# Optimization experiments

Hardware: AMD Instinct MI355X
Metric: run time of the kernel (lower is better)

The kernel has to match this reference:

```python
import jax, jax.numpy as jnp
import numpy as np

HIDDEN_DIM = 256
N = 8192


def setup_inputs() -> dict:
    key = jax.random.key(0)
    k1, k2, k3, k4 = jax.random.split(key, 4)
    img = jax.random.normal(k1, (N, HIDDEN_DIM), dtype=jnp.float32)
    text = jax.random.normal(k2, (N, HIDDEN_DIM), dtype=jnp.float32)
    # nn.Linear(hidden_dim, hidden_dim, bias=False) weights, shape [out, in]
    scale = 1.0 / np.sqrt(HIDDEN_DIM)
    Wq = jax.random.uniform(k3, (HIDDEN_DIM, HIDDEN_DIM), dtype=jnp.float32, minval=-scale, maxval=scale)
    Wk = jax.random.uniform(k4, (HIDDEN_DIM, HIDDEN_DIM), dtype=jnp.float32, minval=-scale, maxval=scale)
    return {"img": img, "text": text, "Wq": Wq, "Wk": Wk}


def reference(img, text, Wq, Wk):
    d = img.shape[-1]
    norm_fact = 1.0 / jnp.sqrt(jnp.asarray(d, dtype=img.dtype))
    Q = img @ Wq.T                       # [N, D]
    K = text @ Wk.T                      # [N, D]
    scores = Q @ K.T                     # [N, N]
    # softmax over dim=1 (keys), then scaled by 1/sqrt(D)
    attn = jax.nn.softmax(scores, axis=1) * norm_fact
    out_img = attn @ img                 # [N, D]
    out_text = attn @ text               # [N, D]
    return (out_img, out_text)
```

## Files before the change

kernel.cpp:

```cpp
#include <hip/hip_runtime.h>

typedef unsigned short ushort_t;
typedef unsigned int uint_t;
typedef __attribute__((ext_vector_type(8))) short short8;
typedef __attribute__((ext_vector_type(8))) _Float16 half8;
typedef __attribute__((ext_vector_type(4))) _Float16 half4;
typedef __attribute__((ext_vector_type(4))) float float4v;

#define MFMA_BF16(a, b, c) __builtin_amdgcn_mfma_f32_16x16x32_bf16((a), (b), (c), 0, 0, 0)
#define MFMA_F16(a, b, c) __builtin_amdgcn_mfma_f32_16x16x32_f16((a), (b), (c), 0, 0, 0)

#define NQ 8192
#define DIM 256
#define DV 512

__device__ __forceinline__ ushort_t f2bf(float x) {
  union { float f; uint_t u; } v; v.f = x;
  return (ushort_t)((v.u + 0x7fffu + ((v.u >> 16) & 1u)) >> 16);
}
__device__ __forceinline__ float bf2f(ushort_t b) {
  union { uint_t u; float f; } v; v.u = ((uint_t)b) << 16;
  return v.f;
}

__device__ __forceinline__ half8 cvt8h(const float* p) {
  float4v a = *(const float4v*)p;
  float4v b = *(const float4v*)(p + 4);
  half8 r;
  r[0] = (_Float16)a[0]; r[1] = (_Float16)a[1];
  r[2] = (_Float16)a[2]; r[3] = (_Float16)a[3];
  r[4] = (_Float16)b[0]; r[5] = (_Float16)b[1];
  r[6] = (_Float16)b[2]; r[7] = (_Float16)b[3];
  return r;
}

__device__ __forceinline__ half8 as_h8(short8 s) {
  union { short8 s; half8 h; } u; u.s = s; return u.h;
}

__device__ __forceinline__ void load_lds_16(const void* g, void* l) {
  __builtin_amdgcn_global_load_lds(
      (const __attribute__((address_space(1))) uint_t*)g,
      (__attribute__((address_space(3))) uint_t*)l, 16, 0, 0);
}

__device__ __forceinline__ void barrier_vm0_lgkm0() {
  asm volatile("s_waitcnt vmcnt(0) lgkmcnt(0)\ns_barrier" ::: "memory");
}
__device__ __forceinline__ void barrier_lgkm0() {
  asm volatile("s_waitcnt lgkmcnt(0)\ns_barrier" ::: "memory");
}

__global__ __launch_bounds__(256, 2) void pre_kernel(
    const float* __restrict__ img, const float* __restrict__ text,
    const float* __restrict__ Wq, const float* __restrict__ Wk,
    _Float16* __restrict__ Qh, _Float16* __restrict__ Kh,
    ushort_t* __restrict__ Vt) {
  __shared__ float tile[64][65];
  const int bid = blockIdx.x;
  const int tid = threadIdx.x;
  if (bid < 1024) {
    const int bx = bid & 127;
    const int by = (bid >> 7) & 3;
    const int bz = bid >> 9;
    const int lane = tid & 63;
    const int wv = tid >> 6;
    const int l16 = lane & 15;
    const int quad = lane >> 4;
    const float* A = bz ? text : img;
    const float* W = bz ? Wk : Wq;
    _Float16* C = bz ? Kh : Qh;
    const int row = bx * 64 + wv * 16 + l16;
    const int colbase = by * 64;

    float4v acc[4];
#pragma unroll
    for (int c = 0; c < 4; ++c) acc[c] = (float4v){0.f, 0.f, 0.f, 0.f};
#pragma unroll
    for (int f = 0; f < 8; ++f) {
      const int k0 = f * 32 + quad * 8;
      half8 af = cvt8h(A + (size_t)row * DIM + k0);
#pragma unroll
      for (int c = 0; c < 4; ++c) {
        half8 bfr = cvt8h(W + (size_t)(colbase + c * 16 + l16) * DIM + k0);
        acc[c] = MFMA_F16(af, bfr, acc[c]);
      }
    }
    const int rbase = bx * 64 + wv * 16 + quad * 4;
#pragma unroll
    for (int c = 0; c < 4; ++c)
#pragma unroll
      for (int r = 0; r < 4; ++r)
        C[(size_t)(rbase + r) * DIM + colbase + c * 16 + l16] = (_Float16)acc[c][r];
  } else {
    const int vb = bid - 1024;
    const int n0 = (vb & 127) * 64;
    const int c0 = (vb >> 7) * 64;
    const float* src = (c0 < 256) ? img : text;
    const int cc0 = (c0 < 256) ? c0 : (c0 - 256);
#pragma unroll
    for (int i = 0; i < 4; ++i) {
      const int r = i * 16 + (tid >> 4);
      const int c = (tid & 15) * 4;
      *(float4v*)&tile[r][c] = *(const float4v*)(src + (size_t)(n0 + r) * DIM + cc0 + c);
    }
    __syncthreads();
    const int c = tid >> 2;
    const int seg = tid & 3;
    ushort_t tmp[16];
#pragma unroll
    for (int t = 0; t < 16; ++t) tmp[t] = f2bf(tile[seg * 16 + t][c]);
    ushort_t* dst = Vt + (size_t)(c0 + c) * NQ + n0 + seg * 16;
    *(short8*)dst = *(short8*)&tmp[0];
    *(short8*)(dst + 8) = *(short8*)&tmp[8];
  }
}

__device__ __forceinline__ void stage_K(const _Float16* __restrict__ Kh, int k0,
                                        ushort_t* dst, int tid, int wv) {
#pragma unroll
  for (int i = 0; i < 4; ++i) {
    const int chunk = i * 256 + tid;
    const int n = chunk >> 5;
    const int cs = (chunk & 31) ^ (n & 7);
    load_lds_16(Kh + (size_t)(k0 + n) * DIM + cs * 8,
                (char*)dst + (i * 256 + wv * 64) * 16);
  }
}
__device__ __forceinline__ void stage_V(const ushort_t* __restrict__ Vt, int k0,
                                        ushort_t* dst, int tid, int wv) {
#pragma unroll
  for (int i = 0; i < 8; ++i) {
    const int chunk = i * 256 + tid;
    const int vrow = chunk >> 2;
    const int dc = (chunk & 3) ^ ((vrow >> 1) & 3);
    load_lds_16(Vt + (size_t)vrow * NQ + k0 + dc * 8,
                (char*)dst + (i * 256 + wv * 64) * 16);
  }
}

__global__ __launch_bounds__(256, 2) void attn_kernel(
    const _Float16* __restrict__ Qh, const _Float16* __restrict__ Kh,
    const ushort_t* __restrict__ Vt, _Float16* __restrict__ pacc,
    float* __restrict__ pdenom, int kps, int ks) {
  extern __shared__ __align__(16) ushort_t smem[];
  ushort_t* ldsV = smem + 16384;

  const int tid = threadIdx.x;
  const int lane = tid & 63;
  const int wv = tid >> 6;
  const int l16 = lane & 15;
  const int quad = lane >> 4;
  const int id = blockIdx.x;
  const int split = id & (ks - 1);
  const int qtile = id / ks;
  const int kbeg = split * kps;
  const int sw2 = (l16 >> 1) & 3;
  const int swk = l16 & 7;

  short8 qf[8];
  {
    const _Float16* qptr = Qh + (size_t)(qtile * 64 + wv * 16 + l16) * DIM;
#pragma unroll
    for (int f = 0; f < 8; ++f)
      qf[f] = *(const short8*)(qptr + f * 32 + quad * 8);
  }

  float4v acc[4][8];
#pragma unroll
  for (int m = 0; m < 4; ++m)
#pragma unroll
    for (int c = 0; c < 8; ++c) acc[m][c] = (float4v){0.f, 0.f, 0.f, 0.f};
  float dacc[4] = {0.f, 0.f, 0.f, 0.f};

  const int ntiles = kps >> 5;

  stage_K(Kh, kbeg, smem, tid, wv);
  stage_V(Vt, kbeg, ldsV, tid, wv);

  for (int t = 0; t < ntiles; ++t) {
    const ushort_t* Kt = smem + (t & 1) * 8192;
    barrier_vm0_lgkm0();
    if (t + 1 < ntiles)
      stage_K(Kh, kbeg + (t + 1) * 32, smem + ((t + 1) & 1) * 8192, tid, wv);

    if (t > 0) {
      const ushort_t* Pprev = smem + 32768 + ((t - 1) & 1) * 2048;
      short8 pa[4];
#pragma unroll
      for (int m = 0; m < 4; ++m)
        pa[m] = *(const short8*)(Pprev + (m * 16 + l16) * 32 + (quad ^ sw2) * 8);
#pragma unroll
      for (int c = 0; c < 8; ++c) {
        const int vcol = (wv * 8 + c) * 16 + l16;
        short8 vb = *(const short8*)(ldsV + vcol * 32 + (quad ^ sw2) * 8);
#pragma unroll
        for (int m = 0; m < 4; ++m)
          acc[m][c] = MFMA_BF16(pa[m], vb, acc[m][c]);
      }
    }

    float4v s0 = (float4v){0.f, 0.f, 0.f, 0.f};
    float4v s1 = (float4v){0.f, 0.f, 0.f, 0.f};
#pragma unroll
    for (int f = 0; f < 8; ++f) {
      const int cs = ((f * 4 + quad) ^ swk) * 8;
      short8 kb0 = *(const short8*)(Kt + l16 * DIM + cs);
      short8 kb1 = *(const short8*)(Kt + (l16 + 16) * DIM + cs);
      s0 = MFMA_F16(as_h8(qf[f]), as_h8(kb0), s0);
      s1 = MFMA_F16(as_h8(qf[f]), as_h8(kb1), s1);
    }

    barrier_lgkm0();
    if (t >= 1) stage_V(Vt, kbeg + t * 32, ldsV, tid, wv);

    ushort_t* Pcur = smem + 32768 + (t & 1) * 2048;
    ushort_t pb0[4], pb1[4];
#pragma unroll
    for (int r = 0; r < 4; ++r) {
      pb0[r] = f2bf(__expf(s0[r]));
      pb1[r] = f2bf(__expf(s1[r]));
    }
#pragma unroll
    for (int r = 0; r < 4; ++r) {
      float ts = bf2f(pb0[r]) + bf2f(pb1[r]);
      ts += __shfl_xor(ts, 1);
      ts += __shfl_xor(ts, 2);
      ts += __shfl_xor(ts, 4);
      ts += __shfl_xor(ts, 8);
      dacc[r] += ts;
    }
#pragma unroll
    for (int r = 0; r < 4; ++r) {
      const int rb = wv * 16 + quad * 4 + r;
      const int swp = (rb >> 1) & 3;
      Pcur[rb * 32 + ((l16 >> 3) ^ swp) * 8 + (l16 & 7)] = pb0[r];
      Pcur[rb * 32 + ((2 + (l16 >> 3)) ^ swp) * 8 + (l16 & 7)] = pb1[r];
    }
  }

  barrier_vm0_lgkm0();
  {
    const ushort_t* Pprev = smem + 32768 + ((ntiles - 1) & 1) * 2048;
    short8 pa[4];
#pragma unroll
    for (int m = 0; m < 4; ++m)
      pa[m] = *(const short8*)(Pprev + (m * 16 + l16) * 32 + (quad ^ sw2) * 8);
#pragma unroll
    for (int c = 0; c < 8; ++c) {
      const int vcol = (wv * 8 + c) * 16 + l16;
      short8 vb = *(const short8*)(ldsV + vcol * 32 + (quad ^ sw2) * 8);
#pragma unroll
      for (int m = 0; m < 4; ++m)
        acc[m][c] = MFMA_BF16(pa[m], vb, acc[m][c]);
    }
  }

  barrier_lgkm0();
  float* ldsD = (float*)smem;
  if (l16 == 0) {
#pragma unroll
    for (int r = 0; r < 4; ++r)
      ldsD[wv * 16 + quad * 4 + r] = dacc[r];
  }
  barrier_lgkm0();

  _Float16* pout = pacc + (size_t)split * ((size_t)NQ * DV);
#pragma unroll
  for (int m = 0; m < 4; ++m) {
    float invd[4];
#pragma unroll
    for (int r = 0; r < 4; ++r) invd[r] = 1.0f / ldsD[m * 16 + quad * 4 + r];
    const int rowbase = qtile * 64 + m * 16 + quad * 4;
#pragma unroll
    for (int c = 0; c < 8; ++c) {
      const int col = (wv * 8 + c) * 16 + l16;
#pragma unroll
      for (int r = 0; r < 4; ++r)
        pout[(size_t)(rowbase + r) * DV + col] = (_Float16)(acc[m][c][r] * invd[r]);
    }
  }
  if (l16 == 0) {
    const int rowbase = qtile * 64 + wv * 16 + quad * 4;
#pragma unroll
    for (int r = 0; r < 4; ++r)
      pdenom[split * NQ + rowbase + r] = dacc[r];
  }
}

__global__ __launch_bounds__(256) void combine_kernel(
    const _Float16* __restrict__ pacc, const float* __restrict__ pdenom,
    float* __restrict__ out, int ks) {
  const int idx = blockIdx.x * 256 + threadIdx.x;
  const int n = idx >> 7;
  const int c4 = (idx & 127) << 2;
  float4v s = (float4v){0.f, 0.f, 0.f, 0.f};
  float dsum = 0.f;
  for (int sp = 0; sp < ks; ++sp) {
    const float d = pdenom[sp * NQ + n];
    half4 x = *(const half4*)(pacc + (size_t)sp * ((size_t)NQ * DV) + (size_t)n * DV + c4);
    s[0] += d * (float)x[0];
    s[1] += d * (float)x[1];
    s[2] += d * (float)x[2];
    s[3] += d * (float)x[3];
    dsum += d;
  }
  const float scale = 1.0f / (16.0f * dsum);
  s *= scale;
  float* dst = (c4 < 256) ? (out + (size_t)n * DIM + c4)
                          : (out + (size_t)NQ * DIM + (size_t)n * DIM + (c4 - 256));
  *(float4v*)dst = s;
}

extern "C" void kernel_launch(void* const* d_in, const int* in_sizes, int n_in,
                              void* d_out, int out_size, void* d_ws, size_t ws_size,
                              hipStream_t stream) {
  const float* img = (const float*)d_in[0];
  const float* text = (const float*)d_in[1];
  const float* Wq = (const float*)d_in[2];
  const float* Wk = (const float*)d_in[3];
  float* out = (float*)d_out;
  char* ws = (char*)d_ws;

  _Float16* Qh = (_Float16*)ws;
  _Float16* Kh = (_Float16*)(ws + ((size_t)4 << 20));
  ushort_t* Vt = (ushort_t*)(ws + ((size_t)8 << 20));
  const size_t accsz = (size_t)NQ * DV * sizeof(_Float16);
  const size_t base = (size_t)16 << 20;

  int ks = 4;
  if (ws_size < base + 4 * (accsz + NQ * sizeof(float))) ks = 2;
  _Float16* pacc = (_Float16*)(ws + base);
  float* pdenom = (float*)(ws + base + (size_t)ks * accsz);

  hipLaunchKernelGGL(pre_kernel, dim3(2048), dim3(256), 0, stream,
                     img, text, Wq, Wk, Qh, Kh, Vt);
  hipLaunchKernelGGL(attn_kernel, dim3(128 * ks), dim3(256),
                     36864 * sizeof(ushort_t), stream,
                     Qh, Kh, Vt, pacc, pdenom, NQ / ks, ks);
  hipLaunchKernelGGL(combine_kernel, dim3((NQ * DV / 4) / 256), dim3(256), 0, stream,
                     pacc, pdenom, out, ks);
}
```

Measured before the change: 263.3 us.

## Double attention block to 8 waves and compute row sums via MFMA with ones

Raises the attention block from 4 to 8 waves: each wave now owns a 16-key half of the QK score tile and a 64-column slice of the PV output, which halves per-wave accumulator registers and doubles waves per block. The softmax denominator is no longer summed with a chain of cross-lane shuffles; instead waves 0-3 add an extra bf16 MFMA of the P tile against a vector of ones. This trades shuffle and VALU work for one more MFMA per tile and more threads sharing the same barriers, with 512-thread blocks aiming for higher occupancy.

```diff
diff --git a/kernel.cpp b/kernel.cpp
--- a/kernel.cpp
+++ b/kernel.cpp
@@ -17,10 +17,6 @@
 __device__ __forceinline__ ushort_t f2bf(float x) {
   union { float f; uint_t u; } v; v.f = x;
   return (ushort_t)((v.u + 0x7fffu + ((v.u >> 16) & 1u)) >> 16);
-}
-__device__ __forceinline__ float bf2f(ushort_t b) {
-  union { uint_t u; float f; } v; v.u = ((uint_t)b) << 16;
-  return v.f;
 }
 
 __device__ __forceinline__ half8 cvt8h(const float* p) {
@@ -119,27 +115,27 @@
 __device__ __forceinline__ void stage_K(const _Float16* __restrict__ Kh, int k0,
                                         ushort_t* dst, int tid, int wv) {
 #pragma unroll
-  for (int i = 0; i < 4; ++i) {
-    const int chunk = i * 256 + tid;
+  for (int i = 0; i < 2; ++i) {
+    const int chunk = i * 512 + tid;
     const int n = chunk >> 5;
     const int cs = (chunk & 31) ^ (n & 7);
     load_lds_16(Kh + (size_t)(k0 + n) * DIM + cs * 8,
-                (char*)dst + (i * 256 + wv * 64) * 16);
+                (char*)dst + (i * 512 + wv * 64) * 16);
   }
 }
 __device__ __forceinline__ void stage_V(const ushort_t* __restrict__ Vt, int k0,
                                         ushort_t* dst, int tid, int wv) {
 #pragma unroll
-  for (int i = 0; i < 8; ++i) {
-    const int chunk = i * 256 + tid;
+  for (int i = 0; i < 4; ++i) {
+    const int chunk = i * 512 + tid;
     const int vrow = chunk >> 2;
     const int dc = (chunk & 3) ^ ((vrow >> 1) & 3);
     load_lds_16(Vt + (size_t)vrow * NQ + k0 + dc * 8,
-                (char*)dst + (i * 256 + wv * 64) * 16);
-  }
-}
-
-__global__ __launch_bounds__(256, 2) void attn_kernel(
+                (char*)dst + (i * 512 + wv * 64) * 16);
+  }
+}
+
+__global__ __launch_bounds__(512, 4) void attn_kernel(
     const _Float16* __restrict__ Qh, const _Float16* __restrict__ Kh,
     const ushort_t* __restrict__ Vt, _Float16* __restrict__ pacc,
     float* __restrict__ pdenom, int kps, int ks) {
@@ -150,7 +146,9 @@
   const int lane = tid & 63;
   const int wv = tid >> 6;
   const int l16 = lane & 15;
-  const int quad = lane >> 4;
+  const int quad = (lane >> 4) & 3;
+  const int qblk = wv & 3;
+  const int kh = wv >> 2;
   const int id = blockIdx.x;
   const int split = id & (ks - 1);
   const int qtile = id / ks;
@@ -158,20 +156,22 @@
   const int sw2 = (l16 >> 1) & 3;
   const int swk = l16 & 7;
 
+  const short8 ones = {0x3F80, 0x3F80, 0x3F80, 0x3F80, 0x3F80, 0x3F80, 0x3F80, 0x3F80};
+
   short8 qf[8];
   {
-    const _Float16* qptr = Qh + (size_t)(qtile * 64 + wv * 16 + l16) * DIM;
+    const _Float16* qptr = Qh + (size_t)(qtile * 64 + qblk * 16 + l16) * DIM;
 #pragma unroll
     for (int f = 0; f < 8; ++f)
       qf[f] = *(const short8*)(qptr + f * 32 + quad * 8);
   }
 
-  float4v acc[4][8];
+  float4v acc[4][4];
 #pragma unroll
   for (int m = 0; m < 4; ++m)
 #pragma unroll
-    for (int c = 0; c < 8; ++c) acc[m][c] = (float4v){0.f, 0.f, 0.f, 0.f};
-  float dacc[4] = {0.f, 0.f, 0.f, 0.f};
+    for (int c = 0; c < 4; ++c) acc[m][c] = (float4v){0.f, 0.f, 0.f, 0.f};
+  float4v dden = (float4v){0.f, 0.f, 0.f, 0.f};
 
   const int ntiles = kps >> 5;
 
@@ -191,51 +191,35 @@
       for (int m = 0; m < 4; ++m)
         pa[m] = *(const short8*)(Pprev + (m * 16 + l16) * 32 + (quad ^ sw2) * 8);
 #pragma unroll
-      for (int c = 0; c < 8; ++c) {
-        const int vcol = (wv * 8 + c) * 16 + l16;
+      for (int c = 0; c < 4; ++c) {
+        const int vcol = (wv * 4 + c) * 16 + l16;
         short8 vb = *(const short8*)(ldsV + vcol * 32 + (quad ^ sw2) * 8);
 #pragma unroll
         for (int m = 0; m < 4; ++m)
           acc[m][c] = MFMA_BF16(pa[m], vb, acc[m][c]);
       }
-    }
-
-    float4v s0 = (float4v){0.f, 0.f, 0.f, 0.f};
-    float4v s1 = (float4v){0.f, 0.f, 0.f, 0.f};
+      if (wv < 4) dden = MFMA_BF16(pa[wv], ones, dden);
+    }
+
+    float4v s = (float4v){0.f, 0.f, 0.f, 0.f};
 #pragma unroll
     for (int f = 0; f < 8; ++f) {
       const int cs = ((f * 4 + quad) ^ swk) * 8;
-      short8 kb0 = *(const short8*)(Kt + l16 * DIM + cs);
-      short8 kb1 = *(const short8*)(Kt + (l16 + 16) * DIM + cs);
-      s0 = MFMA_F16(as_h8(qf[f]), as_h8(kb0), s0);
-      s1 = MFMA_F16(as_h8(qf[f]), as_h8(kb1), s1);
+      short8 kb = *(const short8*)(Kt + (kh * 16 + l16) * DIM + cs);
+      s = MFMA_F16(as_h8(qf[f]), as_h8(kb), s);
     }
 
     barrier_lgkm0();
     if (t >= 1) stage_V(Vt, kbeg + t * 32, ldsV, tid, wv);
 
     ushort_t* Pcur = smem + 32768 + (t & 1) * 2048;
-    ushort_t pb0[4], pb1[4];
 #pragma unroll
     for (int r = 0; r < 4; ++r) {
-      pb0[r] = f2bf(__expf(s0[r]));
-      pb1[r] = f2bf(__expf(s1[r]));
-    }
-#pragma unroll
-    for (int r = 0; r < 4; ++r) {
-      float ts = bf2f(pb0[r]) + bf2f(pb1[r]);
-      ts += __shfl_xor(ts, 1);
-      ts += __shfl_xor(ts, 2);
-      ts += __shfl_xor(ts, 4);
-      ts += __shfl_xor(ts, 8);
-      dacc[r] += ts;
-    }
-#pragma unroll
-    for (int r = 0; r < 4; ++r) {
-      const int rb = wv * 16 + quad * 4 + r;
-      const int swp = (rb >> 1) & 3;
-      Pcur[rb * 32 + ((l16 >> 3) ^ swp) * 8 + (l16 & 7)] = pb0[r];
-      Pcur[rb * 32 + ((2 + (l16 >> 3)) ^ swp) * 8 + (l16 & 7)] = pb1[r];
+      const ushort_t p = f2bf(__expf(s[r]));
+      const int rb = qblk * 16 + quad * 4 + r;
+      const int kc = kh * 2 + (l16 >> 3);
+      const int pos = kc ^ ((rb >> 1) & 3);
+      Pcur[rb * 32 + pos * 8 + (l16 & 7)] = p;
     }
   }
 
@@ -247,21 +231,22 @@
     for (int m = 0; m < 4; ++m)
       pa[m] = *(const short8*)(Pprev + (m * 16 + l16) * 32 + (quad ^ sw2) * 8);
 #pragma unroll
-    for (int c = 0; c < 8; ++c) {
-      const int vcol = (wv * 8 + c) * 16 + l16;
+    for (int c = 0; c < 4; ++c) {
+      const int vcol = (wv * 4 + c) * 16 + l16;
       short8 vb = *(const short8*)(ldsV + vcol * 32 + (quad ^ sw2) * 8);
 #pragma unroll
       for (int m = 0; m < 4; ++m)
         acc[m][c] = MFMA_BF16(pa[m], vb, acc[m][c]);
     }
+    if (wv < 4) dden = MFMA_BF16(pa[wv], ones, dden);
   }
 
   barrier_lgkm0();
   float* ldsD = (float*)smem;
-  if (l16 == 0) {
+  if (wv < 4 && l16 == 0) {
 #pragma unroll
     for (int r = 0; r < 4; ++r)
-      ldsD[wv * 16 + quad * 4 + r] = dacc[r];
+      ldsD[wv * 16 + quad * 4 + r] = dden[r];
   }
   barrier_lgkm0();
 
@@ -273,18 +258,18 @@
     for (int r = 0; r < 4; ++r) invd[r] = 1.0f / ldsD[m * 16 + quad * 4 + r];
     const int rowbase = qtile * 64 + m * 16 + quad * 4;
 #pragma unroll
-    for (int c = 0; c < 8; ++c) {
-      const int col = (wv * 8 + c) * 16 + l16;
+    for (int c = 0; c < 4; ++c) {
+      const int col = (wv * 4 + c) * 16 + l16;
 #pragma unroll
       for (int r = 0; r < 4; ++r)
         pout[(size_t)(rowbase + r) * DV + col] = (_Float16)(acc[m][c][r] * invd[r]);
     }
   }
-  if (l16 == 0) {
+  if (wv < 4 && l16 == 0) {
     const int rowbase = qtile * 64 + wv * 16 + quad * 4;
 #pragma unroll
     for (int r = 0; r < 4; ++r)
-      pdenom[split * NQ + rowbase + r] = dacc[r];
+      pdenom[split * NQ + rowbase + r] = dden[r];
   }
 }
 
@@ -335,7 +320,7 @@
 
   hipLaunchKernelGGL(pre_kernel, dim3(2048), dim3(256), 0, stream,
                      img, text, Wq, Wk, Qh, Kh, Vt);
-  hipLaunchKernelGGL(attn_kernel, dim3(128 * ks), dim3(256),
+  hipLaunchKernelGGL(attn_kernel, dim3(128 * ks), dim3(512),
                      36864 * sizeof(ushort_t), stream,
                      Qh, Kh, Vt, pacc, pdenom, NQ / ks, ks);
   hipLaunchKernelGGL(combine_kernel, dim3((NQ * DV / 4) / 256), dim3(256), 0, stream,
```

Measured after the change: 806.6 us. 206% more time.

## Load V fragments directly into registers and compute row sums with MFMA

Applied to the files above, without the earlier changes.

V tiles are no longer staged through LDS. Each wave loads its own V fragments from global memory straight into registers, one tile ahead. The softmax denominator now comes from an extra MFMA against a ones vector, which replaces the shuffle reductions, and one barrier is removed. LDS use drops from about 72KB to 40KB, which may allow higher occupancy. In exchange, global V loads are strided, uncoalesced row accesses without LDS reuse, which adds register pressure and memory latency on the critical path.

```diff
diff --git a/kernel.cpp b/kernel.cpp
--- a/kernel.cpp
+++ b/kernel.cpp
@@ -17,10 +17,6 @@
 __device__ __forceinline__ ushort_t f2bf(float x) {
   union { float f; uint_t u; } v; v.f = x;
   return (ushort_t)((v.u + 0x7fffu + ((v.u >> 16) & 1u)) >> 16);
-}
-__device__ __forceinline__ float bf2f(ushort_t b) {
-  union { uint_t u; float f; } v; v.u = ((uint_t)b) << 16;
-  return v.f;
 }
 
 __device__ __forceinline__ half8 cvt8h(const float* p) {
@@ -127,24 +123,12 @@
                 (char*)dst + (i * 256 + wv * 64) * 16);
   }
 }
-__device__ __forceinline__ void stage_V(const ushort_t* __restrict__ Vt, int k0,
-                                        ushort_t* dst, int tid, int wv) {
-#pragma unroll
-  for (int i = 0; i < 8; ++i) {
-    const int chunk = i * 256 + tid;
-    const int vrow = chunk >> 2;
-    const int dc = (chunk & 3) ^ ((vrow >> 1) & 3);
-    load_lds_16(Vt + (size_t)vrow * NQ + k0 + dc * 8,
-                (char*)dst + (i * 256 + wv * 64) * 16);
-  }
-}
 
 __global__ __launch_bounds__(256, 2) void attn_kernel(
     const _Float16* __restrict__ Qh, const _Float16* __restrict__ Kh,
     const ushort_t* __restrict__ Vt, _Float16* __restrict__ pacc,
     float* __restrict__ pdenom, int kps, int ks) {
   extern __shared__ __align__(16) ushort_t smem[];
-  ushort_t* ldsV = smem + 16384;
 
   const int tid = threadIdx.x;
   const int lane = tid & 63;
@@ -158,6 +142,8 @@
   const int sw2 = (l16 >> 1) & 3;
   const int swk = l16 & 7;
 
+  const short8 ones = {0x3F80, 0x3F80, 0x3F80, 0x3F80, 0x3F80, 0x3F80, 0x3F80, 0x3F80};
+
   short8 qf[8];
   {
     const _Float16* qptr = Qh + (size_t)(qtile * 64 + wv * 16 + l16) * DIM;
@@ -171,12 +157,17 @@
   for (int m = 0; m < 4; ++m)
 #pragma unroll
     for (int c = 0; c < 8; ++c) acc[m][c] = (float4v){0.f, 0.f, 0.f, 0.f};
-  float dacc[4] = {0.f, 0.f, 0.f, 0.f};
+  float4v dden = (float4v){0.f, 0.f, 0.f, 0.f};
 
   const int ntiles = kps >> 5;
 
   stage_K(Kh, kbeg, smem, tid, wv);
-  stage_V(Vt, kbeg, ldsV, tid, wv);
+  short8 vreg[8];
+#pragma unroll
+  for (int c = 0; c < 8; ++c) {
+    const int vcol = (wv * 8 + c) * 16 + l16;
+    vreg[c] = *(const short8*)(Vt + (size_t)vcol * NQ + kbeg + quad * 8);
+  }
 
   for (int t = 0; t < ntiles; ++t) {
     const ushort_t* Kt = smem + (t & 1) * 8192;
@@ -185,18 +176,22 @@
       stage_K(Kh, kbeg + (t + 1) * 32, smem + ((t + 1) & 1) * 8192, tid, wv);
 
     if (t > 0) {
-      const ushort_t* Pprev = smem + 32768 + ((t - 1) & 1) * 2048;
+      const ushort_t* Pprev = smem + 16384 + ((t - 1) & 1) * 2048;
       short8 pa[4];
 #pragma unroll
       for (int m = 0; m < 4; ++m)
         pa[m] = *(const short8*)(Pprev + (m * 16 + l16) * 32 + (quad ^ sw2) * 8);
 #pragma unroll
       for (int c = 0; c < 8; ++c) {
+#pragma unroll
+        for (int m = 0; m < 4; ++m)
+          acc[m][c] = MFMA_BF16(pa[m], vreg[c], acc[m][c]);
+      }
+      dden = MFMA_BF16(pa[wv], ones, dden);
+#pragma unroll
+      for (int c = 0; c < 8; ++c) {
         const int vcol = (wv * 8 + c) * 16 + l16;
-        short8 vb = *(const short8*)(ldsV + vcol * 32 + (quad ^ sw2) * 8);
-#pragma unroll
-        for (int m = 0; m < 4; ++m)
-          acc[m][c] = MFMA_BF16(pa[m], vb, acc[m][c]);
+        vreg[c] = *(const short8*)(Vt + (size_t)vcol * NQ + (kbeg + t * 32) + quad * 8);
       }
     }
 
@@ -211,49 +206,32 @@
       s1 = MFMA_F16(as_h8(qf[f]), as_h8(kb1), s1);
     }
 
-    barrier_lgkm0();
-    if (t >= 1) stage_V(Vt, kbeg + t * 32, ldsV, tid, wv);
-
-    ushort_t* Pcur = smem + 32768 + (t & 1) * 2048;
-    ushort_t pb0[4], pb1[4];
+    ushort_t* Pcur = smem + 16384 + (t & 1) * 2048;
 #pragma unroll
     for (int r = 0; r < 4; ++r) {
-      pb0[r] = f2bf(__expf(s0[r]));
-      pb1[r] = f2bf(__expf(s1[r]));
-    }
-#pragma unroll
-    for (int r = 0; r < 4; ++r) {
-      float ts = bf2f(pb0[r]) + bf2f(pb1[r]);
-      ts += __shfl_xor(ts, 1);
-      ts += __shfl_xor(ts, 2);
-      ts += __shfl_xor(ts, 4);
-      ts += __shfl_xor(ts, 8);
-      dacc[r] += ts;
-    }
-#pragma unroll
-    for (int r = 0; r < 4; ++r) {
+      const ushort_t p0 = f2bf(__expf(s0[r]));
+      const ushort_t p1 = f2bf(__expf(s1[r]));
       const int rb = wv * 16 + quad * 4 + r;
       const int swp = (rb >> 1) & 3;
-      Pcur[rb * 32 + ((l16 >> 3) ^ swp) * 8 + (l16 & 7)] = pb0[r];
-      Pcur[rb * 32 + ((2 + (l16 >> 3)) ^ swp) * 8 + (l16 & 7)] = pb1[r];
+      Pcur[rb * 32 + ((l16 >> 3) ^ swp) * 8 + (l16 & 7)] = p0;
+      Pcur[rb * 32 + ((2 + (l16 >> 3)) ^ swp) * 8 + (l16 & 7)] = p1;
     }
   }
 
   barrier_vm0_lgkm0();
   {
-    const ushort_t* Pprev = smem + 32768 + ((ntiles - 1) & 1) * 2048;
+    const ushort_t* Pprev = smem + 16384 + ((ntiles - 1) & 1) * 2048;
     short8 pa[4];
 #pragma unroll
     for (int m = 0; m < 4; ++m)
       pa[m] = *(const short8*)(Pprev + (m * 16 + l16) * 32 + (quad ^ sw2) * 8);
 #pragma unroll
     for (int c = 0; c < 8; ++c) {
-      const int vcol = (wv * 8 + c) * 16 + l16;
-      short8 vb = *(const short8*)(ldsV + vcol * 32 + (quad ^ sw2) * 8);
 #pragma unroll
       for (int m = 0; m < 4; ++m)
-        acc[m][c] = MFMA_BF16(pa[m], vb, acc[m][c]);
-    }
+        acc[m][c] = MFMA_BF16(pa[m], vreg[c], acc[m][c]);
+    }
+    dden = MFMA_BF16(pa[wv], ones, dden);
   }
 
   barrier_lgkm0();
@@ -261,7 +239,7 @@
   if (l16 == 0) {
 #pragma unroll
     for (int r = 0; r < 4; ++r)
-      ldsD[wv * 16 + quad * 4 + r] = dacc[r];
+      ldsD[wv * 16 + quad * 4 + r] = dden[r];
   }
   barrier_lgkm0();
 
@@ -284,7 +262,7 @@
     const int rowbase = qtile * 64 + wv * 16 + quad * 4;
 #pragma unroll
     for (int r = 0; r < 4; ++r)
-      pdenom[split * NQ + rowbase + r] = dacc[r];
+      pdenom[split * NQ + rowbase + r] = dden[r];
   }
 }
 
@@ -336,7 +314,7 @@
   hipLaunchKernelGGL(pre_kernel, dim3(2048), dim3(256), 0, stream,
                      img, text, Wq, Wk, Qh, Kh, Vt);
   hipLaunchKernelGGL(attn_kernel, dim3(128 * ks), dim3(256),
-                     36864 * sizeof(ushort_t), stream,
+                     20480 * sizeof(ushort_t), stream,
                      Qh, Kh, Vt, pacc, pdenom, NQ / ks, ks);
   hipLaunchKernelGGL(combine_kernel, dim3((NQ * DV / 4) / 256), dim3(256), 0, stream,
                      pacc, pdenom, out, ks);
```

Result: slower. 415.5 us (+57.8%).
